# Kernel optimization log

Hardware: AMD Instinct MI355X
Metric: run time of the kernel (lower is better)

## Reference

```python
import jax, jax.numpy as jnp
import numpy as np


def setup_inputs() -> dict:
    key = jax.random.key(0)
    L, N, Q, C = 6, 64, 64, 256
    hs_pair = jax.random.normal(key, (L, N, Q, C), dtype=jnp.float32)
    return {"hs_pair": hs_pair}


def _merge_step(centers):
    # centers: [L, N, Q, C] -> [L, N, Q-1, C]
    L, N, Q, C = centers.shape
    # pairwise Euclidean distance via gram matrix (avoids [L,N,Q,Q,C] diff tensor)
    sq = jnp.sum(centers * centers, axis=-1)                      # [L,N,Q]
    gram = jnp.einsum('lnqc,lnpc->lnqp', centers, centers)        # [L,N,Q,Q]
    d2 = sq[..., :, None] + sq[..., None, :] - 2.0 * gram
    dist = jnp.sqrt(jnp.maximum(d2, 0.0))                         # [L,N,Q,Q]
    dist = dist + jnp.max(dist) * jnp.eye(Q, dtype=dist.dtype)
    idx = jnp.argmin(dist.reshape(L, N, Q * Q), axis=2)           # [L,N]
    x, y = idx // Q, idx % Q                                      # row-major argmin => x < y
    cx = jnp.take_along_axis(centers, x[:, :, None, None], axis=2)[:, :, 0]  # [L,N,C]
    cy = jnp.take_along_axis(centers, y[:, :, None, None], axis=2)[:, :, 0]  # [L,N,C]
    merged = (cx + cy) * 0.5
    last = centers[:, :, -1]                                      # [L,N,C]
    qr = jnp.arange(Q)
    mask_x = (qr[None, None, :] == x[:, :, None])[..., None]      # [L,N,Q,1]
    mask_y = (qr[None, None, :] == y[:, :, None])[..., None]
    centers = jnp.where(mask_x, merged[:, :, None, :], centers)
    centers = jnp.where(mask_y, last[:, :, None, :], centers)
    return centers[:, :, :-1]


def reference(hs_pair):
    centers = hs_pair
    Q0 = centers.shape[2]
    # Q-2 sequential merges; each iteration has a distinct static shape,
    # so a Python loop (unrolled under jit) is the correct structure.
    for _ in range(Q0 - 2):
        centers = _merge_step(centers)
    return centers  # [L, N, 2, C]
```

## Files before the change

kernel.cpp:

```cpp
#include <hip/hip_runtime.h>
#include <stdint.h>

#define NSLICE 384
#define QMAX   64
#define CDIM   256
#define NTHR   512

#define SW(r,c) ((r)*QMAX + ((c)^(r)))
#define INF_F  __int_as_float(0x7F800000)

__device__ __forceinline__ float dpp_sum64(float v) {
#define DPP_ADD(c) v += __int_as_float(__builtin_amdgcn_update_dpp(0, __float_as_int(v), c, 0xf, 0xf, true))
    DPP_ADD(0x111);
    DPP_ADD(0x112);
    DPP_ADD(0x114);
    DPP_ADD(0x118);
    DPP_ADD(0x142);
    DPP_ADD(0x143);
#undef DPP_ADD
    return v;
}

template<int CTRL>
__device__ __forceinline__ unsigned dpp_min_step(unsigned v) {
    unsigned o = (unsigned)__builtin_amdgcn_update_dpp((int)v, (int)v, CTRL, 0xf, 0xf, false);
    return v < o ? v : o;
}

__device__ __forceinline__ unsigned wave_min_bcast(unsigned v) {
    v = dpp_min_step<0x111>(v);
    v = dpp_min_step<0x112>(v);
    v = dpp_min_step<0x114>(v);
    v = dpp_min_step<0x118>(v);
    v = dpp_min_step<0x142>(v);
    v = dpp_min_step<0x143>(v);
    return (unsigned)__builtin_amdgcn_readlane((int)v, 63);
}

__device__ __forceinline__ unsigned oct_min_all(unsigned v) {
    v = dpp_min_step<0xB1>(v);
    v = dpp_min_step<0x4E>(v);
    v = dpp_min_step<0x124>(v);
    return v;
}

__launch_bounds__(NTHR, 4)
__global__ void hca_kernel(const float* __restrict__ in, float* __restrict__ out) {
    __shared__ __align__(16) float cen[QMAX * CDIM];
    __shared__ __align__(16) float dist[QMAX * QMAX];
    unsigned long long* const scratch = (unsigned long long*)(dist + 63 * QMAX);

    const int tid  = threadIdx.x;
    const int lane = tid & 63;
    const int w    = tid >> 6;
    const int slice = blockIdx.x;
    const float* src = in + (size_t)slice * (QMAX * CDIM);
    float* dst = out + (size_t)slice * (2 * CDIM);

    {
        const float4* s4 = (const float4*)src;
        float4* c4 = (float4*)cen;
        #pragma unroll
        for (int i = 0; i < (QMAX * CDIM / 4) / NTHR; ++i)
            c4[tid + i * NTHR] = s4[tid + i * NTHR];
    }
    __syncthreads();

    {
        float4 A[8];
        #pragma unroll
        for (int r = 0; r < 8; ++r)
            A[r] = ((const float4*)(cen + (w + 8 * r) * CDIM))[lane];

        #pragma unroll
        for (int r = 0; r < 8; ++r) {
            float t = A[r].x * A[r].x;
            t = fmaf(A[r].y, A[r].y, t); t = fmaf(A[r].z, A[r].z, t); t = fmaf(A[r].w, A[r].w, t);
            float s = dpp_sum64(t);
            if (lane == 63) dist[(w + 8 * r) * QMAX] = s;
        }
        __syncthreads();

        float sqq[8];
        #pragma unroll
        for (int r = 0; r < 8; ++r) sqq[r] = dist[(w + 8 * r) * QMAX];
        for (int p = 1; p < QMAX; ++p) {
            const float4 b = ((const float4*)(cen + p * CDIM))[lane];
            const float sqp = dist[p * QMAX];
            #pragma unroll
            for (int r = 0; r < 8; ++r) {
                const int q = w + 8 * r;
                if (q < p) {
                    float t = A[r].x * b.x;
                    t = fmaf(A[r].y, b.y, t); t = fmaf(A[r].z, b.z, t); t = fmaf(A[r].w, b.w, t);
                    float s = dpp_sum64(t);
                    if (lane == 63) {
                        float d2 = sqq[r] + sqp - 2.0f * s;
                        float d  = sqrtf(fmaxf(d2, 0.0f));
                        dist[SW(q, p)] = d;
                        dist[SW(p, q)] = d;
                    }
                }
            }
        }
    }
    __syncthreads();

    auto chunk_min = [&](const float4& dv, unsigned& part) {
        unsigned u0 = __float_as_uint(dv.x), u1 = __float_as_uint(dv.y);
        unsigned u2 = __float_as_uint(dv.z), u3 = __float_as_uint(dv.w);
        unsigned m01 = u0 < u1 ? u0 : u1;
        unsigned m23 = u2 < u3 ? u2 : u3;
        unsigned m = m01 < m23 ? m01 : m23;
        part = part < m ? part : m;
    };
    auto chunk_idx = [&](int i, const float4& dv, unsigned g, unsigned& bi) {
        const int rr  = 4 * i + (lane >> 4);
        const int rb  = rr * 64;
        const int cc0 = (lane & 15) * 4;
        #pragma unroll
        for (int e = 0; e < 4; ++e) {
            unsigned db  = __float_as_uint((&dv.x)[e]);
            unsigned idx = (unsigned)(rb + ((cc0 + e) ^ rr));
            if (db == g) bi = idx < bi ? idx : bi;
        }
    };

    unsigned flat0, d0bits;
    {
        unsigned part = 0xFFFFFFFFu;
        float4 dv[16];
        #pragma unroll
        for (int i = 0; i < 16; ++i) {
            dv[i] = ((const float4*)dist)[i * 64 + lane];
            chunk_min(dv[i], part);
        }
        d0bits = wave_min_bcast(part);
        unsigned bi = 0xFFFFFFFFu;
        #pragma unroll
        for (int i = 0; i < 16; ++i) chunk_idx(i, dv[i], d0bits, bi);
        flat0 = wave_min_bcast(bi);
    }
    __syncthreads();

    for (int Q = QMAX; Q > 2; --Q) {
        int x, y; unsigned dxyb;
        if (Q == QMAX) {
            x = (int)(flat0 >> 6); y = (int)(flat0 & 63); dxyb = d0bits;
        } else {
            unsigned long long k = scratch[lane & 7];
            unsigned hi = (unsigned)(k >> 32), lo = (unsigned)k;
            unsigned ghi = oct_min_all(hi);
            unsigned c2  = (hi == ghi) ? lo : 0xFFFFFFFFu;
            unsigned flat = oct_min_all(c2);
            x = (int)((flat >> 6) & 63); y = (int)(flat & 63);
            dxyb = ghi;
        }

        if (w == 0) {
            const int p = lane;
            const bool act = (p < Q - 1) && (p != x);
            const int p_old = (p == y) ? (Q - 1) : p;
            float dxp = 0.0f, dyp = 0.0f;
            if (act) {
                dxp = dist[SW(x, p_old)];
                dyp = dist[SW(y, p_old)];
            }
            const bool mv = (y != Q - 1) && (p < Q - 1) && (p != x) && (p != y);
            float rowQ1 = 0.0f, colQ1 = 0.0f;
            if (mv) {
                rowQ1 = dist[SW(Q - 1, p)];
                colQ1 = dist[SW(p, Q - 1)];
            }
            const float dxy = __uint_as_float(dxyb);
            float t = 0.5f * (dxp * dxp + dyp * dyp) - 0.25f * (dxy * dxy);
            float d = sqrtf(fmaxf(t, 0.0f));
            if (mv) {
                dist[SW(y, p)] = rowQ1;
                dist[SW(p, y)] = colQ1;
            }
            if (p < Q) {
                dist[SW(Q - 1, p)] = INF_F;
                dist[SW(p, Q - 1)] = INF_F;
            }
            if (act) {
                dist[SW(x, p)] = d;
                dist[SW(p, x)] = d;
            }
        }
        if (w == 1) {
            const float4 cx = ((const float4*)(cen + x * CDIM))[lane];
            const float4 cy = ((const float4*)(cen + y * CDIM))[lane];
            const float4 cq = ((const float4*)(cen + (Q - 1) * CDIM))[lane];
            float4 m;
            m.x = (cx.x + cy.x) * 0.5f; m.y = (cx.y + cy.y) * 0.5f;
            m.z = (cx.z + cy.z) * 0.5f; m.w = (cx.w + cy.w) * 0.5f;
            ((float4*)(cen + x * CDIM))[lane] = m;
            if (y != Q - 1)
                ((float4*)(cen + y * CDIM))[lane] = cq;
        }
        __syncthreads();

        if (Q > 3) {
            const int Qs = Q - 1;
            unsigned part = 0xFFFFFFFFu;
            float4 dv0, dv1;
            const bool live0 = (4 * w < Qs);
            const bool live1 = (4 * (w + 8) < Qs);
            if (live0) {
                dv0 = ((const float4*)dist)[w * 64 + lane];
                chunk_min(dv0, part);
            }
            if (live1) {
                dv1 = ((const float4*)dist)[(w + 8) * 64 + lane];
                if (w + 8 == 15 && lane >= 48) {
                    dv1.x = INF_F; dv1.y = INF_F; dv1.z = INF_F; dv1.w = INF_F;
                }
                chunk_min(dv1, part);
            }
            unsigned g = wave_min_bcast(part);
            unsigned bi = 0xFFFFFFFFu;
            if (live0) chunk_idx(w, dv0, g, bi);
            if (live1) chunk_idx(w + 8, dv1, g, bi);
            unsigned bidx = wave_min_bcast(bi);
            if (lane == 0) scratch[w] = ((unsigned long long)g << 32) | bidx;
        }
        __syncthreads();
    }

    for (int i = tid; i < 2 * CDIM; i += NTHR)
        dst[i] = cen[i];
}

extern "C" void kernel_launch(void* const* d_in, const int* in_sizes, int n_in,
                              void* d_out, int out_size, void* d_ws, size_t ws_size,
                              hipStream_t stream) {
    (void)in_sizes; (void)n_in; (void)d_ws; (void)ws_size; (void)out_size;
    const float* in = (const float*)d_in[0];
    float* out = (float*)d_out;
    hca_kernel<<<NSLICE, NTHR, 0, stream>>>(in, out);
}
```

Measured before the change: 129.2 us.

## Overlap argmin search with distance update to halve barriers per merge step

Restructures the merge loop so each iteration needs one barrier instead of two. Waves 1-7 read the distance matrix before the update and mask out the rows and columns of x, y and Q-1, while wave 0 performs the update and computes the minima of the new row x and the moved row y. Partial argmin results go to double-buffered scratch slots and are combined with a 16-lane DPP min reduction. The cost is extra masking work, more complex bookkeeping, and a risk of tie-break or correctness mismatches with the reference argmin order.

```diff
diff --git a/kernel.cpp b/kernel.cpp
--- a/kernel.cpp
+++ b/kernel.cpp
@@ -37,10 +37,11 @@
     return (unsigned)__builtin_amdgcn_readlane((int)v, 63);
 }
 
-__device__ __forceinline__ unsigned oct_min_all(unsigned v) {
+__device__ __forceinline__ unsigned grp16_min(unsigned v) {
     v = dpp_min_step<0xB1>(v);
     v = dpp_min_step<0x4E>(v);
     v = dpp_min_step<0x124>(v);
+    v = dpp_min_step<0x128>(v);
     return v;
 }
 
@@ -48,7 +49,7 @@
 __global__ void hca_kernel(const float* __restrict__ in, float* __restrict__ out) {
     __shared__ __align__(16) float cen[QMAX * CDIM];
     __shared__ __align__(16) float dist[QMAX * QMAX];
-    unsigned long long* const scratch = (unsigned long long*)(dist + 63 * QMAX);
+    unsigned long long* const SCR = (unsigned long long*)(dist + 63 * QMAX);
 
     const int tid  = threadIdx.x;
     const int lane = tid & 63;
@@ -143,87 +144,157 @@
     }
     __syncthreads();
 
-    for (int Q = QMAX; Q > 2; --Q) {
-        int x, y; unsigned dxyb;
-        if (Q == QMAX) {
-            x = (int)(flat0 >> 6); y = (int)(flat0 & 63); dxyb = d0bits;
-        } else {
-            unsigned long long k = scratch[lane & 7];
-            unsigned hi = (unsigned)(k >> 32), lo = (unsigned)k;
-            unsigned ghi = oct_min_all(hi);
-            unsigned c2  = (hi == ghi) ? lo : 0xFFFFFFFFu;
-            unsigned flat = oct_min_all(c2);
-            x = (int)((flat >> 6) & 63); y = (int)(flat & 63);
-            dxyb = ghi;
-        }
-
+    {
+        const int Qm1 = 63;
+        const int x = (int)(flat0 >> 6), y = (int)(flat0 & 63);
+        const float dxy = __uint_as_float(d0bits);
         if (w == 0) {
             const int p = lane;
-            const bool act = (p < Q - 1) && (p != x);
-            const int p_old = (p == y) ? (Q - 1) : p;
+            const bool act = (p < Qm1) && (p != x);
+            const int p_old = (p == y) ? Qm1 : p;
             float dxp = 0.0f, dyp = 0.0f;
-            if (act) {
-                dxp = dist[SW(x, p_old)];
-                dyp = dist[SW(y, p_old)];
-            }
-            const bool mv = (y != Q - 1) && (p < Q - 1) && (p != x) && (p != y);
+            if (act) { dxp = dist[SW(x, p_old)]; dyp = dist[SW(y, p_old)]; }
+            const bool mv = (y != Qm1) && (p < Qm1) && (p != x) && (p != y);
             float rowQ1 = 0.0f, colQ1 = 0.0f;
-            if (mv) {
-                rowQ1 = dist[SW(Q - 1, p)];
-                colQ1 = dist[SW(p, Q - 1)];
-            }
-            const float dxy = __uint_as_float(dxyb);
+            if (mv) { rowQ1 = dist[SW(Qm1, p)]; colQ1 = dist[SW(p, Qm1)]; }
             float t = 0.5f * (dxp * dxp + dyp * dyp) - 0.25f * (dxy * dxy);
             float d = sqrtf(fmaxf(t, 0.0f));
-            if (mv) {
-                dist[SW(y, p)] = rowQ1;
-                dist[SW(p, y)] = colQ1;
-            }
-            if (p < Q) {
-                dist[SW(Q - 1, p)] = INF_F;
-                dist[SW(p, Q - 1)] = INF_F;
-            }
-            if (act) {
-                dist[SW(x, p)] = d;
-                dist[SW(p, x)] = d;
-            }
+            if (mv) { dist[SW(y, p)] = rowQ1; dist[SW(p, y)] = colQ1; }
+            if (p < QMAX) dist[SW(p, Qm1)] = INF_F;
+            if (act) { dist[SW(x, p)] = d; dist[SW(p, x)] = d; }
         }
         if (w == 1) {
             const float4 cx = ((const float4*)(cen + x * CDIM))[lane];
             const float4 cy = ((const float4*)(cen + y * CDIM))[lane];
-            const float4 cq = ((const float4*)(cen + (Q - 1) * CDIM))[lane];
+            const float4 cq = ((const float4*)(cen + Qm1 * CDIM))[lane];
             float4 m;
             m.x = (cx.x + cy.x) * 0.5f; m.y = (cx.y + cy.y) * 0.5f;
             m.z = (cx.z + cy.z) * 0.5f; m.w = (cx.w + cy.w) * 0.5f;
             ((float4*)(cen + x * CDIM))[lane] = m;
-            if (y != Q - 1)
-                ((float4*)(cen + y * CDIM))[lane] = cq;
+            if (y != Qm1) ((float4*)(cen + y * CDIM))[lane] = cq;
         }
         __syncthreads();
 
-        if (Q > 3) {
-            const int Qs = Q - 1;
+        if (w == 0) {
+            if (lane < 16) {
+                if (lane == 0 || lane >= 10) SCR[lane] = ~0ull;
+                if (lane == 0 || lane >= 8)  SCR[16 + lane] = ~0ull;
+            }
+        } else {
             unsigned part = 0xFFFFFFFFu;
-            float4 dv0, dv1;
-            const bool live0 = (4 * w < Qs);
-            const bool live1 = (4 * (w + 8) < Qs);
-            if (live0) {
-                dv0 = ((const float4*)dist)[w * 64 + lane];
-                chunk_min(dv0, part);
-            }
-            if (live1) {
-                dv1 = ((const float4*)dist)[(w + 8) * 64 + lane];
-                if (w + 8 == 15 && lane >= 48) {
-                    dv1.x = INF_F; dv1.y = INF_F; dv1.z = INF_F; dv1.w = INF_F;
-                }
-                chunk_min(dv1, part);
+            const int c0 = w - 1, c1 = w + 6;
+            const int c2 = (w == 3) ? 14 : ((w == 4) ? 15 : -1);
+            float4 v0 = ((const float4*)dist)[c0 * 64 + lane]; chunk_min(v0, part);
+            float4 v1 = ((const float4*)dist)[c1 * 64 + lane]; chunk_min(v1, part);
+            float4 v2;
+            if (c2 >= 0) {
+                v2 = ((const float4*)dist)[c2 * 64 + lane];
+                if (c2 == 15 && lane >= 48) { v2.x = INF_F; v2.y = INF_F; v2.z = INF_F; v2.w = INF_F; }
+                chunk_min(v2, part);
             }
             unsigned g = wave_min_bcast(part);
             unsigned bi = 0xFFFFFFFFu;
-            if (live0) chunk_idx(w, dv0, g, bi);
-            if (live1) chunk_idx(w + 8, dv1, g, bi);
+            chunk_idx(c0, v0, g, bi);
+            chunk_idx(c1, v1, g, bi);
+            if (c2 >= 0) chunk_idx(c2, v2, g, bi);
             unsigned bidx = wave_min_bcast(bi);
-            if (lane == 0) scratch[w] = ((unsigned long long)g << 32) | bidx;
+            if (lane == 0) SCR[16 + w] = ((unsigned long long)g << 32) | bidx;
+        }
+        __syncthreads();
+    }
+
+    for (int Q = 63; Q > 2; --Q) {
+        const int k = 64 - Q;
+        const unsigned long long* bufc = SCR + ((k & 1) ? 16 : 0);
+        unsigned long long* const bufn = SCR + ((k & 1) ? 0 : 16);
+        const int Qm1 = Q - 1;
+
+        float4 v0, v1, v2;
+        int c0 = 0, c1 = 0, c2 = -1;
+        bool l0 = false, l1 = false, l2 = false;
+        if (Q > 3 && w != 0) {
+            c0 = w - 1; c1 = w + 6; c2 = (w == 3) ? 14 : ((w == 4) ? 15 : -1);
+            l0 = (4 * c0 < Qm1); l1 = (4 * c1 < Qm1); l2 = (c2 >= 0) && (4 * c2 < Qm1);
+            if (l0) v0 = ((const float4*)dist)[c0 * 64 + lane];
+            if (l1) v1 = ((const float4*)dist)[c1 * 64 + lane];
+            if (l2) v2 = ((const float4*)dist)[c2 * 64 + lane];
+        }
+
+        const unsigned long long kk = bufc[lane & 15];
+        const unsigned hi = (unsigned)(kk >> 32), lo = (unsigned)kk;
+        const unsigned g  = grp16_min(hi);
+        const unsigned fl = grp16_min((hi == g) ? lo : 0xFFFFFFFFu);
+        const int x = (int)((fl >> 6) & 63), y = (int)(fl & 63);
+        const float dxy = __uint_as_float(g);
+
+        if (Q > 3) {
+            if (w == 0) {
+                const int p = lane;
+                const bool act = (p < Qm1) && (p != x);
+                const int p_old = (p == y) ? Qm1 : p;
+                float dxp = 0.0f, dyp = 0.0f;
+                if (act) { dxp = dist[SW(x, p_old)]; dyp = dist[SW(y, p_old)]; }
+                const bool mv = (y != Qm1) && (p < Qm1) && (p != x) && (p != y);
+                float rowQ1 = 0.0f, colQ1 = 0.0f;
+                if (mv) { rowQ1 = dist[SW(Qm1, p)]; colQ1 = dist[SW(p, Qm1)]; }
+                float t = 0.5f * (dxp * dxp + dyp * dyp) - 0.25f * (dxy * dxy);
+                float d = sqrtf(fmaxf(t, 0.0f));
+                if (mv) { dist[SW(y, p)] = rowQ1; dist[SW(p, y)] = colQ1; }
+                if (p < Q) { dist[SW(Qm1, p)] = INF_F; dist[SW(p, Qm1)] = INF_F; }
+                if (act) { dist[SW(x, p)] = d; dist[SW(p, x)] = d; }
+                unsigned h1 = act ? __float_as_uint(d) : 0xFFFFFFFFu;
+                unsigned g1 = wave_min_bcast(h1);
+                unsigned r1 = 0xFFFFFFFFu;
+                if (act && h1 == g1) {
+                    int a = x < p ? x : p, b = x < p ? p : x;
+                    r1 = (unsigned)(a * 64 + b);
+                }
+                unsigned i1 = wave_min_bcast(r1);
+                unsigned h2 = mv ? __float_as_uint(colQ1) : 0xFFFFFFFFu;
+                unsigned g2 = wave_min_bcast(h2);
+                unsigned r2 = 0xFFFFFFFFu;
+                if (mv && h2 == g2) {
+                    int a = p < y ? p : y, b = p < y ? y : p;
+                    r2 = (unsigned)(a * 64 + b);
+                }
+                unsigned i2 = wave_min_bcast(r2);
+                if (lane == 0) {
+                    bufn[8] = ((unsigned long long)g1 << 32) | i1;
+                    bufn[9] = ((unsigned long long)g2 << 32) | i2;
+                }
+            } else {
+                auto mask4 = [&](int j, float4& vv) {
+                    const int rr = 4 * j + (lane >> 4);
+                    const bool rb = (rr == x) | (rr == y) | (rr == Qm1) | (rr == 63);
+                    const int cc0 = (lane & 15) * 4;
+                    #pragma unroll
+                    for (int e = 0; e < 4; ++e) {
+                        const int c = (cc0 + e) ^ rr;
+                        if (rb | (c == x) | (c == y) | (c == Qm1)) (&vv.x)[e] = INF_F;
+                    }
+                };
+                unsigned part = 0xFFFFFFFFu;
+                if (l0) { mask4(c0, v0); chunk_min(v0, part); }
+                if (l1) { mask4(c1, v1); chunk_min(v1, part); }
+                if (l2) { mask4(c2, v2); chunk_min(v2, part); }
+                unsigned gs = wave_min_bcast(part);
+                unsigned bi = 0xFFFFFFFFu;
+                if (l0) chunk_idx(c0, v0, gs, bi);
+                if (l1) chunk_idx(c1, v1, gs, bi);
+                if (l2) chunk_idx(c2, v2, gs, bi);
+                unsigned bidx = wave_min_bcast(bi);
+                if (lane == 0) bufn[w] = ((unsigned long long)gs << 32) | bidx;
+            }
+        }
+        if (w == 1) {
+            const float4 cx = ((const float4*)(cen + x * CDIM))[lane];
+            const float4 cy4 = ((const float4*)(cen + y * CDIM))[lane];
+            const float4 cq = ((const float4*)(cen + Qm1 * CDIM))[lane];
+            float4 m;
+            m.x = (cx.x + cy4.x) * 0.5f; m.y = (cx.y + cy4.y) * 0.5f;
+            m.z = (cx.z + cy4.z) * 0.5f; m.w = (cx.w + cy4.w) * 0.5f;
+            ((float4*)(cen + x * CDIM))[lane] = m;
+            if (y != Qm1) ((float4*)(cen + y * CDIM))[lane] = cq;
         }
         __syncthreads();
     }
```

Result: slower. 145.3 us (+12.4%).
